# Optimization experiments

Measured on AMD Instinct MI355X. Metric: run time of the kernel, lower is better.

Reference implementation:

```python
import jax, jax.numpy as jnp
import numpy as np

N, E, IN_DIM, HID = 50000, 800000, 512, 256
EPS = 1e-5


def _gat_layer(x, W, a_src, a_dst, b, src, dst, n, heads, ch):
    # x: [N, F_in] -> h: [N, H, C]
    h = (x @ W).reshape(n, heads, ch)
    alpha_src = jnp.sum(h * a_src, axis=-1)  # [N, H]
    alpha_dst = jnp.sum(h * a_dst, axis=-1)  # [N, H]
    e = jax.nn.leaky_relu(alpha_src[src] + alpha_dst[dst], negative_slope=0.2)  # [E', H]
    # segment softmax over incoming edges of each destination node
    m = jax.ops.segment_max(e, dst, num_segments=n)  # [N, H]
    ex = jnp.exp(e - m[dst])
    den = jax.ops.segment_sum(ex, dst, num_segments=n)  # [N, H]
    alpha = ex / den[dst]
    out = jax.ops.segment_sum(alpha[:, :, None] * h[src], dst, num_segments=n)  # [N, H, C]
    return out.reshape(n, heads * ch) + b


def _layer_norm(x, w, b):
    mu = jnp.mean(x, axis=-1, keepdims=True)
    var = jnp.mean(jnp.square(x - mu), axis=-1, keepdims=True)
    return (x - mu) * jax.lax.rsqrt(var + EPS) * w + b


def setup_inputs() -> dict:
    key = jax.random.key(0)
    ks = jax.random.split(key, 16)
    d = {}
    d['x'] = jax.random.normal(ks[0], (N, IN_DIM), dtype=jnp.float32)
    d['edge_index'] = jax.random.randint(ks[1], (2, E), 0, N, dtype=jnp.int32)
    s = 0.05
    # layer 0: GATConv(512, 64, heads=4)
    d['W0'] = jax.random.normal(ks[2], (IN_DIM, HID), dtype=jnp.float32) * s
    d['as0'] = jax.random.normal(ks[3], (4, 64), dtype=jnp.float32) * s
    d['ad0'] = jax.random.normal(ks[4], (4, 64), dtype=jnp.float32) * s
    d['b0'] = jnp.zeros((HID,), dtype=jnp.float32)
    d['lnw0'] = jnp.ones((HID,), dtype=jnp.float32)
    d['lnb0'] = jnp.zeros((HID,), dtype=jnp.float32)
    # layer 1: GATConv(256, 64, heads=4)
    d['W1'] = jax.random.normal(ks[5], (HID, HID), dtype=jnp.float32) * s
    d['as1'] = jax.random.normal(ks[6], (4, 64), dtype=jnp.float32) * s
    d['ad1'] = jax.random.normal(ks[7], (4, 64), dtype=jnp.float32) * s
    d['b1'] = jnp.zeros((HID,), dtype=jnp.float32)
    d['lnw1'] = jnp.ones((HID,), dtype=jnp.float32)
    d['lnb1'] = jnp.zeros((HID,), dtype=jnp.float32)
    # layer 2: GATConv(256, 256, heads=1)
    d['W2'] = jax.random.normal(ks[8], (HID, HID), dtype=jnp.float32) * s
    d['as2'] = jax.random.normal(ks[9], (1, HID), dtype=jnp.float32) * s
    d['ad2'] = jax.random.normal(ks[10], (1, HID), dtype=jnp.float32) * s
    d['b2'] = jnp.zeros((HID,), dtype=jnp.float32)
    d['lnw2'] = jnp.ones((HID,), dtype=jnp.float32)
    d['lnb2'] = jnp.zeros((HID,), dtype=jnp.float32)
    return d


def reference(x, edge_index, W0, as0, ad0, b0, lnw0, lnb0,
              W1, as1, ad1, b1, lnw1, lnb1,
              W2, as2, ad2, b2, lnw2, lnb2):
    n = x.shape[0]
    loop = jnp.arange(n, dtype=edge_index.dtype)
    src = jnp.concatenate([edge_index[0], loop])  # PyG add_self_loops=True
    dst = jnp.concatenate([edge_index[1], loop])
    h = _gat_layer(x, W0, as0, ad0, b0, src, dst, n, 4, 64)
    h = jax.nn.elu(_layer_norm(h, lnw0, lnb0))
    h = _gat_layer(h, W1, as1, ad1, b1, src, dst, n, 4, 64)
    h = jax.nn.elu(_layer_norm(h, lnw1, lnb1))
    h = _gat_layer(h, W2, as2, ad2, b2, src, dst, n, 1, HID)
    h = jax.nn.elu(_layer_norm(h, lnw2, lnb2))
    return h
```

## Files before the change

### kernel.cpp

```cpp
#include <hip/hip_runtime.h>

#define HID 256
#define EPSV 1e-5f
#define ASTR 72
#define BSTR 40

typedef __bf16 bf16x8 __attribute__((ext_vector_type(8)));
typedef float  floatx4 __attribute__((ext_vector_type(4)));

static __device__ __forceinline__ ushort f2bf(float f) {
  union { float f; unsigned int i; } c; c.f = f;
  unsigned int u = c.i;
  u += 0x7FFFu + ((u >> 16) & 1u);
  return (ushort)(u >> 16);
}
static __device__ __forceinline__ float bf2f(ushort u) {
  union { unsigned int i; float f; } c; c.i = ((unsigned int)u) << 16; return c.f;
}

__global__ void count_kernel(const int* __restrict__ ei, int* __restrict__ deg, int E, int tot) {
  int i = blockIdx.x * blockDim.x + threadIdx.x;
  if (i < tot) {
    int dst = (i < E) ? ei[E + i] : (i - E);
    atomicAdd(&deg[dst], 1);
  }
}

__global__ void scanA_kernel(const int* __restrict__ deg, int* __restrict__ incl,
                             int* __restrict__ sums, int n) {
  __shared__ int buf[1024];
  const int t = threadIdx.x;
  const int i = blockIdx.x * 1024 + t;
  int x = (i < n) ? deg[i] : 0;
  buf[t] = x;
  __syncthreads();
  for (int off = 1; off < 1024; off <<= 1) {
    int v = (t >= off) ? buf[t - off] : 0;
    __syncthreads();
    buf[t] += v;
    __syncthreads();
  }
  if (i < n) incl[i] = buf[t];
  if (t == 1023) sums[blockIdx.x] = buf[1023];
}

__global__ void scanB_kernel(int* __restrict__ sums, int* __restrict__ offs, int nblk) {
  __shared__ int buf[256];
  const int t = threadIdx.x;
  int x = (t < nblk) ? sums[t] : 0;
  buf[t] = x;
  __syncthreads();
  for (int off = 1; off < 256; off <<= 1) {
    int v = (t >= off) ? buf[t - off] : 0;
    __syncthreads();
    buf[t] += v;
    __syncthreads();
  }
  if (t < nblk) offs[t] = buf[t] - x;
  if (t == nblk) offs[nblk] = buf[nblk - 1];
}

__global__ void scanC_kernel(const int* __restrict__ deg, const int* __restrict__ incl,
                             const int* __restrict__ offs, int* __restrict__ rp,
                             int* __restrict__ cur, int n, int nblk) {
  const int i = blockIdx.x * 1024 + threadIdx.x;
  if (i < n) {
    int v = offs[blockIdx.x] + incl[i] - deg[i];
    rp[i] = v;
    cur[i] = v;
  }
  if (i == 0) rp[n] = offs[nblk];
}

__global__ void scatter_kernel(const int* __restrict__ ei, int* __restrict__ cur,
                               int* __restrict__ csr, int E, int tot) {
  int i = blockIdx.x * blockDim.x + threadIdx.x;
  if (i < tot) {
    int src = (i < E) ? ei[i] : (i - E);
    int dst = (i < E) ? ei[E + i] : (i - E);
    int pos = atomicAdd(&cur[dst], 1);
    csr[pos] = src;
  }
}

__global__ void transpose_kernel(const float* __restrict__ W, ushort* __restrict__ Wt, int K) {
  int i = blockIdx.x * blockDim.x + threadIdx.x;
  if (i < K * 256) {
    int k = i >> 8, m = i & 255;
    Wt[m * K + k] = f2bf(W[i]);
  }
}

__global__ __launch_bounds__(256) void gemm_kernel(
    const float* __restrict__ A, const ushort* __restrict__ Bt,
    ushort* __restrict__ hb, int nrows, int K) {
  __shared__ ushort At[128 * ASTR];
  __shared__ ushort Bs[128 * BSTR];
  const int tid  = threadIdx.x;
  const int lane = tid & 63;
  const int wave = tid >> 6;
  const int quad = lane >> 4;
  const int m16  = lane & 15;
  const int row0 = blockIdx.x * 128;
  const int col0 = blockIdx.y * 128;
  const int wm = (wave >> 1) * 64;
  const int wn = (wave & 1) * 64;

  floatx4 acc[4][4];
  #pragma unroll
  for (int i = 0; i < 4; i++)
    #pragma unroll
    for (int j = 0; j < 4; j++) acc[i][j] = (floatx4){0.f, 0.f, 0.f, 0.f};

  const int arow = tid >> 3;
  const int acol = (tid & 7) * 4;
  const int brow = tid >> 2;
  const int bcol = (tid & 3) * 8;

  for (int k0 = 0; k0 < K; k0 += 32) {
    #pragma unroll
    for (int i = 0; i < 4; i++) {
      int r = arow + 32 * i;
      int ar = min(row0 + r, nrows - 1);
      floatx4 v = *(const floatx4*)(A + (size_t)ar * K + k0 + acol);
      union { ushort us[4]; unsigned long long u64; } ph, pl;
      #pragma unroll
      for (int j = 0; j < 4; j++) {
        ushort hi = f2bf(v[j]);
        ph.us[j] = hi;
        pl.us[j] = f2bf(v[j] - bf2f(hi));
      }
      *(unsigned long long*)&At[r * ASTR + acol]      = ph.u64;
      *(unsigned long long*)&At[r * ASTR + 32 + acol] = pl.u64;
    }
    #pragma unroll
    for (int i = 0; i < 2; i++) {
      int r = brow + 64 * i;
      *(int4*)&Bs[r * BSTR + bcol] =
          *(const int4*)(Bt + (size_t)(col0 + r) * K + k0 + bcol);
    }
    __syncthreads();
    bf16x8 bfr[4];
    #pragma unroll
    for (int j = 0; j < 4; j++)
      bfr[j] = *(const bf16x8*)&Bs[(wn + j * 16 + m16) * BSTR + quad * 8];
    #pragma unroll
    for (int p = 0; p < 2; p++) {
      bf16x8 af[4];
      #pragma unroll
      for (int i = 0; i < 4; i++)
        af[i] = *(const bf16x8*)&At[(wm + i * 16 + m16) * ASTR + p * 32 + quad * 8];
      #pragma unroll
      for (int i = 0; i < 4; i++)
        #pragma unroll
        for (int j = 0; j < 4; j++)
          acc[i][j] = __builtin_amdgcn_mfma_f32_16x16x32_bf16(af[i], bfr[j], acc[i][j], 0, 0, 0);
    }
    __syncthreads();
  }
  #pragma unroll
  for (int i = 0; i < 4; i++) {
    int rbase = row0 + wm + i * 16 + quad * 4;
    #pragma unroll
    for (int j = 0; j < 4; j++) {
      int col = col0 + wn + j * 16 + m16;
      #pragma unroll
      for (int r = 0; r < 4; r++) {
        int row = rbase + r;
        if (row < nrows) hb[(size_t)row * HID + col] = f2bf(acc[i][j][r]);
      }
    }
  }
}

__global__ __launch_bounds__(256) void alpha_kernel(
    const ushort* __restrict__ hb, const float* __restrict__ avs,
    const float* __restrict__ avd, float* __restrict__ asrc,
    float* __restrict__ adst, int H) {
  const int n = blockIdx.x, t = threadIdx.x;
  float hv = bf2f(hb[(size_t)n * HID + t]);
  float s = hv * avs[t];
  float d = hv * avd[t];
  #pragma unroll
  for (int o = 32; o > 0; o >>= 1) { s += __shfl_xor(s, o); d += __shfl_xor(d, o); }
  __shared__ float ls[4], ld_[4];
  int w = t >> 6;
  if ((t & 63) == 0) { ls[w] = s; ld_[w] = d; }
  __syncthreads();
  if (H == 4) {
    if ((t & 63) == 0) { asrc[n * 4 + w] = ls[w]; adst[n * 4 + w] = ld_[w]; }
  } else {
    if (t == 0) {
      asrc[n] = ls[0] + ls[1] + ls[2] + ls[3];
      adst[n] = ld_[0] + ld_[1] + ld_[2] + ld_[3];
    }
  }
}

__global__ __launch_bounds__(128) void agg_ln_kernel(
    const ushort* __restrict__ hb, const float* __restrict__ asrc,
    const float* __restrict__ adst, const int* __restrict__ rp,
    const int* __restrict__ csr,
    const float* __restrict__ bias, const float* __restrict__ lnw,
    const float* __restrict__ lnb, float* __restrict__ out, int H) {
  __shared__ float2 exs[2][64];
  __shared__ float red[2];
  const int nid = blockIdx.x, t = threadIdx.x;
  const int w = t >> 6, lane = t & 63;
  const int h = lane >> 5;
  const int j32 = lane & 31;
  const int head = (H == 4) ? (2 * w + h) : 0;
  const int ch = 128 * w + 2 * lane;
  const float ad = adst[nid * H + head];
  const int beg = rp[nid], end = rp[nid + 1];
  const char* hbase = (const char*)hb + ch * 2;
  float den = 0.f, a0 = 0.f, a1 = 0.f;

  for (int c0 = beg; c0 < end; c0 += 32) {
    const int cnt = min(32, end - c0);
    float ex = 0.f; int soff = 0;
    if (j32 < cnt) {
      int s = csr[c0 + j32];
      soff = s << 9;
      float e = asrc[s * H + head] + ad;
      e = (e > 0.f) ? e : 0.2f * e;
      ex = __expf(fminf(e, 60.f));
    }
    exs[w][lane] = make_float2(ex, __int_as_float(soff));
    float dsum = ex;
    #pragma unroll
    for (int o = 16; o > 0; o >>= 1) dsum += __shfl_xor(dsum, o);
    den += dsum;
    float2 p = exs[w][h * 32];
    for (int j = 0; j < cnt; j++) {
      float2 pn = exs[w][h * 32 + ((j + 1 < cnt) ? j + 1 : j)];
      unsigned int hv = *(const unsigned int*)(hbase + __float_as_int(p.y));
      float f0 = __uint_as_float(hv << 16);
      float f1 = __uint_as_float(hv & 0xffff0000u);
      a0 = fmaf(p.x, f0, a0);
      a1 = fmaf(p.x, f1, a1);
      p = pn;
    }
  }

  const float inv = 1.f / den;
  const float2 bia = *(const float2*)(bias + ch);
  float v0 = a0 * inv + bia.x;
  float v1 = a1 * inv + bia.y;
  float r1 = v0 + v1;
  #pragma unroll
  for (int o = 32; o > 0; o >>= 1) r1 += __shfl_xor(r1, o);
  if (lane == 0) red[w] = r1;
  __syncthreads();
  float mu = (red[0] + red[1]) * (1.f / HID);
  __syncthreads();
  float d0 = v0 - mu, d1 = v1 - mu;
  float r2 = d0 * d0 + d1 * d1;
  #pragma unroll
  for (int o = 32; o > 0; o >>= 1) r2 += __shfl_xor(r2, o);
  if (lane == 0) red[w] = r2;
  __syncthreads();
  float var = (red[0] + red[1]) * (1.f / HID);
  float rstd = rsqrtf(var + EPSV);
  const float2 wv = *(const float2*)(lnw + ch);
  const float2 bv = *(const float2*)(lnb + ch);
  float y0 = d0 * rstd * wv.x + bv.x;
  float y1 = d1 * rstd * wv.y + bv.y;
  float2 o2;
  o2.x = (y0 > 0.f) ? y0 : expm1f(y0);
  o2.y = (y1 > 0.f) ? y1 : expm1f(y1);
  *(float2*)(out + (size_t)nid * HID + ch) = o2;
}

extern "C" void kernel_launch(void* const* d_in, const int* in_sizes, int n_in,
                              void* d_out, int out_size, void* d_ws, size_t ws_size,
                              hipStream_t stream) {
  const float* x  = (const float*)d_in[0];
  const int*   ei = (const int*)d_in[1];
  const float* Wm[3]  = {(const float*)d_in[2], (const float*)d_in[8],  (const float*)d_in[14]};
  const float* Avs[3] = {(const float*)d_in[3], (const float*)d_in[9],  (const float*)d_in[15]};
  const float* Avd[3] = {(const float*)d_in[4], (const float*)d_in[10], (const float*)d_in[16]};
  const float* Bia[3] = {(const float*)d_in[5], (const float*)d_in[11], (const float*)d_in[17]};
  const float* Lnw[3] = {(const float*)d_in[6], (const float*)d_in[12], (const float*)d_in[18]};
  const float* Lnb[3] = {(const float*)d_in[7], (const float*)d_in[13], (const float*)d_in[19]};
  const int n = in_sizes[0] / 512;
  const int E = in_sizes[1] / 2;
  const int tot = E + n;
  const int nblk = (n + 1023) / 1024;

  char* p = (char*)d_ws;
  ushort* hb   = (ushort*)p; p += (size_t)n * HID * 2;
  float*  agg  = (float*)p;  p += (size_t)n * HID * 4;
  ushort* Wt   = (ushort*)p; p += 256 * 512 * 2;
  float*  asrc = (float*)p;  p += (size_t)n * 4 * 4;
  float*  adst = (float*)p;  p += (size_t)n * 4 * 4;
  int* rp   = (int*)p; p += (size_t)(n + 1) * 4;
  int* cur  = (int*)p; p += (size_t)n * 4;
  int* csr  = (int*)p; p += (size_t)tot * 4;
  int* deg  = (int*)p; p += (size_t)n * 4;
  int* incl = (int*)p; p += (size_t)n * 4;
  int* sums = (int*)p; p += (size_t)(nblk + 1) * 4;
  int* offs = (int*)p; p += (size_t)(nblk + 1) * 4;

  hipMemsetAsync(deg, 0, (size_t)n * 4, stream);
  count_kernel<<<(tot + 255) / 256, 256, 0, stream>>>(ei, deg, E, tot);
  scanA_kernel<<<nblk, 1024, 0, stream>>>(deg, incl, sums, n);
  scanB_kernel<<<1, 256, 0, stream>>>(sums, offs, nblk);
  scanC_kernel<<<nblk, 1024, 0, stream>>>(deg, incl, offs, rp, cur, n, nblk);
  scatter_kernel<<<(tot + 255) / 256, 256, 0, stream>>>(ei, cur, csr, E, tot);

  const int KB[3] = {512, 256, 256};
  const int HH[3] = {4, 4, 1};
  const float* Ain = x;
  dim3 gg((n + 127) / 128, 2);
  for (int l = 0; l < 3; l++) {
    transpose_kernel<<<(KB[l] * 256 + 255) / 256, 256, 0, stream>>>(Wm[l], Wt, KB[l]);
    gemm_kernel<<<gg, 256, 0, stream>>>(Ain, Wt, hb, n, KB[l]);
    alpha_kernel<<<n, 256, 0, stream>>>(hb, Avs[l], Avd[l], asrc, adst, HH[l]);
    agg_ln_kernel<<<n, 128, 0, stream>>>(hb, asrc, adst, rp, csr,
                                         Bia[l], Lnw[l], Lnb[l],
                                         (l == 2) ? (float*)d_out : agg, HH[l]);
    Ain = agg;
  }
}
```

Measured before the change: 719.9 us.

## Emit split-bf16 packed activations from aggregation and use one-wave-per-node aggregation

The aggregation+LayerNorm kernel now handles one destination node per wave, four nodes per block, with each lane holding four channels. Block-level reductions become wave shuffles, so the __syncthreads calls go away. For layers 0 and 1 it writes activations as hi/lo bf16 pairs (a 512-wide packed row), and a new GEMM reads these directly. That GEMM runs a K=512 bf16 MFMA loop that reuses the weight tile for both halves, replacing the fp32 activation read and in-GEMM conversion. The change targets less memory traffic and conversion work in the next layer's GEMM and less per-node sync overhead. The hi+lo split keeps near-fp32 accuracy but doubles the MFMA work over K.

```diff
diff --git a/kernel.cpp b/kernel.cpp
--- a/kernel.cpp
+++ b/kernel.cpp
@@ -173,6 +173,69 @@
   }
 }
 
+__global__ __launch_bounds__(256) void gemm_packed_kernel(
+    const ushort* __restrict__ A, const ushort* __restrict__ Bt,
+    ushort* __restrict__ hb, int nrows) {
+  __shared__ ushort At[128 * BSTR];
+  __shared__ ushort Bs[128 * BSTR];
+  const int tid  = threadIdx.x;
+  const int lane = tid & 63;
+  const int wave = tid >> 6;
+  const int quad = lane >> 4;
+  const int m16  = lane & 15;
+  const int row0 = blockIdx.x * 128;
+  const int col0 = blockIdx.y * 128;
+  const int wm = (wave >> 1) * 64;
+  const int wn = (wave & 1) * 64;
+
+  floatx4 acc[4][4];
+  #pragma unroll
+  for (int i = 0; i < 4; i++)
+    #pragma unroll
+    for (int j = 0; j < 4; j++) acc[i][j] = (floatx4){0.f, 0.f, 0.f, 0.f};
+
+  const int srow = tid >> 2;
+  const int scol = (tid & 3) * 8;
+
+  for (int k0 = 0; k0 < 512; k0 += 32) {
+    const int kb = k0 & 255;
+    #pragma unroll
+    for (int i = 0; i < 2; i++) {
+      int r = srow + 64 * i;
+      int ar = min(row0 + r, nrows - 1);
+      *(int4*)&At[r * BSTR + scol] = *(const int4*)(A + (size_t)ar * 512 + k0 + scol);
+      *(int4*)&Bs[r * BSTR + scol] = *(const int4*)(Bt + (size_t)(col0 + r) * 256 + kb + scol);
+    }
+    __syncthreads();
+    bf16x8 af[4], bfr[4];
+    #pragma unroll
+    for (int j = 0; j < 4; j++)
+      bfr[j] = *(const bf16x8*)&Bs[(wn + j * 16 + m16) * BSTR + quad * 8];
+    #pragma unroll
+    for (int i = 0; i < 4; i++)
+      af[i] = *(const bf16x8*)&At[(wm + i * 16 + m16) * BSTR + quad * 8];
+    #pragma unroll
+    for (int i = 0; i < 4; i++)
+      #pragma unroll
+      for (int j = 0; j < 4; j++)
+        acc[i][j] = __builtin_amdgcn_mfma_f32_16x16x32_bf16(af[i], bfr[j], acc[i][j], 0, 0, 0);
+    __syncthreads();
+  }
+  #pragma unroll
+  for (int i = 0; i < 4; i++) {
+    int rbase = row0 + wm + i * 16 + quad * 4;
+    #pragma unroll
+    for (int j = 0; j < 4; j++) {
+      int col = col0 + wn + j * 16 + m16;
+      #pragma unroll
+      for (int r = 0; r < 4; r++) {
+        int row = rbase + r;
+        if (row < nrows) hb[(size_t)row * HID + col] = f2bf(acc[i][j][r]);
+      }
+    }
+  }
+}
+
 __global__ __launch_bounds__(256) void alpha_kernel(
     const ushort* __restrict__ hb, const float* __restrict__ avs,
     const float* __restrict__ avd, float* __restrict__ asrc,
@@ -197,79 +260,92 @@
   }
 }
 
-__global__ __launch_bounds__(128) void agg_ln_kernel(
+__global__ __launch_bounds__(256) void agg_ln_kernel(
     const ushort* __restrict__ hb, const float* __restrict__ asrc,
     const float* __restrict__ adst, const int* __restrict__ rp,
     const int* __restrict__ csr,
     const float* __restrict__ bias, const float* __restrict__ lnw,
-    const float* __restrict__ lnb, float* __restrict__ out, int H) {
-  __shared__ float2 exs[2][64];
-  __shared__ float red[2];
-  const int nid = blockIdx.x, t = threadIdx.x;
+    const float* __restrict__ lnb, ushort* __restrict__ apk,
+    float* __restrict__ fout, int H, int n) {
+  __shared__ float2 exs[4][64];
+  const int t = threadIdx.x;
   const int w = t >> 6, lane = t & 63;
-  const int h = lane >> 5;
-  const int j32 = lane & 31;
-  const int head = (H == 4) ? (2 * w + h) : 0;
-  const int ch = 128 * w + 2 * lane;
-  const float ad = adst[nid * H + head];
+  const int nid = blockIdx.x * 4 + w;
+  if (nid >= n) return;
+  const int CH = (H == 4) ? 16 : 64;
+  const int jj = lane & (CH - 1);
+  const int hh = (H == 4) ? (lane >> 4) : 0;
+  const int ch = 4 * lane;
+  const float ad = adst[nid * H + hh];
   const int beg = rp[nid], end = rp[nid + 1];
   const char* hbase = (const char*)hb + ch * 2;
-  float den = 0.f, a0 = 0.f, a1 = 0.f;
-
-  for (int c0 = beg; c0 < end; c0 += 32) {
-    const int cnt = min(32, end - c0);
-    float ex = 0.f; int soff = 0;
-    if (j32 < cnt) {
-      int s = csr[c0 + j32];
-      soff = s << 9;
-      float e = asrc[s * H + head] + ad;
+  float den = 0.f, a0 = 0.f, a1 = 0.f, a2 = 0.f, a3 = 0.f;
+
+  for (int c0 = beg; c0 < end; c0 += CH) {
+    const int cnt = min(CH, end - c0);
+    int s = (lane < cnt) ? csr[c0 + lane] : 0;
+    s = __shfl(s, jj);
+    float ex = 0.f;
+    if (jj < cnt) {
+      float e = asrc[s * H + hh] + ad;
       e = (e > 0.f) ? e : 0.2f * e;
       ex = __expf(fminf(e, 60.f));
     }
-    exs[w][lane] = make_float2(ex, __int_as_float(soff));
+    exs[w][lane] = make_float2(ex, __int_as_float(s << 9));
     float dsum = ex;
     #pragma unroll
-    for (int o = 16; o > 0; o >>= 1) dsum += __shfl_xor(dsum, o);
+    for (int o = 32; o > 0; o >>= 1)
+      if (o < CH) dsum += __shfl_xor(dsum, o);
     den += dsum;
-    float2 p = exs[w][h * 32];
+    float2 p = exs[w][hh * CH];
     for (int j = 0; j < cnt; j++) {
-      float2 pn = exs[w][h * 32 + ((j + 1 < cnt) ? j + 1 : j)];
-      unsigned int hv = *(const unsigned int*)(hbase + __float_as_int(p.y));
-      float f0 = __uint_as_float(hv << 16);
-      float f1 = __uint_as_float(hv & 0xffff0000u);
-      a0 = fmaf(p.x, f0, a0);
-      a1 = fmaf(p.x, f1, a1);
+      float2 pn = exs[w][hh * CH + ((j + 1 < cnt) ? j + 1 : j)];
+      uint2 hv = *(const uint2*)(hbase + __float_as_int(p.y));
+      a0 = fmaf(p.x, __uint_as_float(hv.x << 16), a0);
+      a1 = fmaf(p.x, __uint_as_float(hv.x & 0xffff0000u), a1);
+      a2 = fmaf(p.x, __uint_as_float(hv.y << 16), a2);
+      a3 = fmaf(p.x, __uint_as_float(hv.y & 0xffff0000u), a3);
       p = pn;
     }
   }
 
   const float inv = 1.f / den;
-  const float2 bia = *(const float2*)(bias + ch);
-  float v0 = a0 * inv + bia.x;
-  float v1 = a1 * inv + bia.y;
-  float r1 = v0 + v1;
+  const floatx4 bia = *(const floatx4*)(bias + ch);
+  float v0 = a0 * inv + bia[0];
+  float v1 = a1 * inv + bia[1];
+  float v2 = a2 * inv + bia[2];
+  float v3 = a3 * inv + bia[3];
+  float r1 = v0 + v1 + v2 + v3;
   #pragma unroll
   for (int o = 32; o > 0; o >>= 1) r1 += __shfl_xor(r1, o);
-  if (lane == 0) red[w] = r1;
-  __syncthreads();
-  float mu = (red[0] + red[1]) * (1.f / HID);
-  __syncthreads();
-  float d0 = v0 - mu, d1 = v1 - mu;
-  float r2 = d0 * d0 + d1 * d1;
+  float mu = r1 * (1.f / HID);
+  float d0 = v0 - mu, d1 = v1 - mu, d2 = v2 - mu, d3 = v3 - mu;
+  float r2 = d0 * d0 + d1 * d1 + d2 * d2 + d3 * d3;
   #pragma unroll
   for (int o = 32; o > 0; o >>= 1) r2 += __shfl_xor(r2, o);
-  if (lane == 0) red[w] = r2;
-  __syncthreads();
-  float var = (red[0] + red[1]) * (1.f / HID);
-  float rstd = rsqrtf(var + EPSV);
-  const float2 wv = *(const float2*)(lnw + ch);
-  const float2 bv = *(const float2*)(lnb + ch);
-  float y0 = d0 * rstd * wv.x + bv.x;
-  float y1 = d1 * rstd * wv.y + bv.y;
-  float2 o2;
-  o2.x = (y0 > 0.f) ? y0 : expm1f(y0);
-  o2.y = (y1 > 0.f) ? y1 : expm1f(y1);
-  *(float2*)(out + (size_t)nid * HID + ch) = o2;
+  float rstd = rsqrtf(r2 * (1.f / HID) + EPSV);
+  const floatx4 wv = *(const floatx4*)(lnw + ch);
+  const floatx4 bv = *(const floatx4*)(lnb + ch);
+  float y0 = d0 * rstd * wv[0] + bv[0];
+  float y1 = d1 * rstd * wv[1] + bv[1];
+  float y2 = d2 * rstd * wv[2] + bv[2];
+  float y3 = d3 * rstd * wv[3] + bv[3];
+  float o0 = (y0 > 0.f) ? y0 : expm1f(y0);
+  float o1 = (y1 > 0.f) ? y1 : expm1f(y1);
+  float o2 = (y2 > 0.f) ? y2 : expm1f(y2);
+  float o3 = (y3 > 0.f) ? y3 : expm1f(y3);
+  if (apk) {
+    union { ushort us[4]; unsigned long long u64; } ph, pl;
+    ushort h0 = f2bf(o0), h1 = f2bf(o1), h2 = f2bf(o2), h3 = f2bf(o3);
+    ph.us[0] = h0; ph.us[1] = h1; ph.us[2] = h2; ph.us[3] = h3;
+    pl.us[0] = f2bf(o0 - bf2f(h0)); pl.us[1] = f2bf(o1 - bf2f(h1));
+    pl.us[2] = f2bf(o2 - bf2f(h2)); pl.us[3] = f2bf(o3 - bf2f(h3));
+    *(unsigned long long*)(apk + (size_t)nid * 512 + ch)       = ph.u64;
+    *(unsigned long long*)(apk + (size_t)nid * 512 + 256 + ch) = pl.u64;
+  } else {
+    floatx4 ov; ov[0] = o0; ov[1] = o1; ov[2] = o2; ov[3] = o3;
+    *(floatx4*)(fout + (size_t)nid * HID + ch) = ov;
+  }
 }
 
 extern "C" void kernel_launch(void* const* d_in, const int* in_sizes, int n_in,
@@ -290,7 +366,7 @@
 
   char* p = (char*)d_ws;
   ushort* hb   = (ushort*)p; p += (size_t)n * HID * 2;
-  float*  agg  = (float*)p;  p += (size_t)n * HID * 4;
+  ushort* apk  = (ushort*)p; p += (size_t)n * 512 * 2;
   ushort* Wt   = (ushort*)p; p += 256 * 512 * 2;
   float*  asrc = (float*)p;  p += (size_t)n * 4 * 4;
   float*  adst = (float*)p;  p += (size_t)n * 4 * 4;
@@ -311,15 +387,17 @@
 
   const int KB[3] = {512, 256, 256};
   const int HH[3] = {4, 4, 1};
-  const float* Ain = x;
   dim3 gg((n + 127) / 128, 2);
   for (int l = 0; l < 3; l++) {
     transpose_kernel<<<(KB[l] * 256 + 255) / 256, 256, 0, stream>>>(Wm[l], Wt, KB[l]);
-    gemm_kernel<<<gg, 256, 0, stream>>>(Ain, Wt, hb, n, KB[l]);
+    if (l == 0)
+      gemm_kernel<<<gg, 256, 0, stream>>>(x, Wt, hb, n, 512);
+    else
+      gemm_packed_kernel<<<gg, 256, 0, stream>>>(apk, Wt, hb, n);
     alpha_kernel<<<n, 256, 0, stream>>>(hb, Avs[l], Avd[l], asrc, adst, HH[l]);
-    agg_ln_kernel<<<n, 128, 0, stream>>>(hb, asrc, adst, rp, csr,
-                                         Bia[l], Lnw[l], Lnb[l],
-                                         (l == 2) ? (float*)d_out : agg, HH[l]);
-    Ain = agg;
-  }
-}
+    agg_ln_kernel<<<(n + 3) / 4, 256, 0, stream>>>(
+        hb, asrc, adst, rp, csr, Bia[l], Lnw[l], Lnb[l],
+        (l < 2) ? apk : (ushort*)nullptr,
+        (l == 2) ? (float*)d_out : (float*)nullptr, HH[l], n);
+  }
+}
```

Result: no change. 728.2 us (+1.1%).
